# Kernel tuning notes

Measured on AMD Instinct MI355X. Metric: run time of the kernel, lower is better.

## Reference

```python
import jax, jax.numpy as jnp
import numpy as np

# Static cluster layout: B graphs, PER atoms each; first NIN are 'inside'
# (aux_ind==0), remaining NOUT are 'outside' periodic images (aux_ind==1).
B, PER, NIN, K = 256, 1024, 256, 32
NOUT = PER - NIN
N = B * PER
R = 6.0        # cutoff radius (Angstrom)
BOX = 32.0     # box side -> ~30 neighbors within R at this density


def setup_inputs() -> dict:
    key = jax.random.key(0)
    pos = jax.random.uniform(key, (N, 3), dtype=jnp.float32) * BOX
    batch = (jnp.arange(N, dtype=jnp.int32) // PER)
    aux_ind = ((jnp.arange(N, dtype=jnp.int32) % PER) >= NIN).astype(jnp.int32)
    return {"pos": pos, "batch": batch, "aux_ind": aux_ind}


def _select_neighbors(d, valid, k):
    """Pick up to k valid candidates per target, lowest candidate index first.
    d: [..., C] distances, valid: [..., C] bool. Returns (idx, mask, dist),
    each [..., k]; padded slots have mask=False and dist=0."""
    C = d.shape[-1]
    order_key = jnp.where(valid, jnp.arange(C, dtype=jnp.int32), C + 1)
    idx = jnp.argsort(order_key, axis=-1)[..., :k]          # [..., k]
    mask = jnp.take_along_axis(valid, idx, axis=-1)
    dist = jnp.where(mask, jnp.take_along_axis(d, idx, axis=-1), 0.0)
    return idx.astype(jnp.int32), mask, dist


def reference(pos, batch, aux_ind):
    # batch/aux_ind are encoded by the static contiguous layout above;
    # they parameterize the same structure torch builds via scatter_add/cumsum.
    pg = pos.reshape(B, PER, 3)
    ins = pg[:, :NIN]            # [B, NIN, 3]  inside (target + intra-conv) nodes
    outs = pg[:, NIN:]           # [B, NOUT, 3] outside (inter-conv) nodes

    # intra edges: inside -> inside, same graph, no self loops
    d_ii = jnp.sqrt(jnp.sum((ins[:, :, None, :] - ins[:, None, :, :]) ** 2, -1))  # [B,NIN,NIN]
    valid_ii = (d_ii < R) & ~jnp.eye(NIN, dtype=bool)
    idx_ii, m_ii, dist_ii = _select_neighbors(d_ii, valid_ii, K)

    # inter edges: outside -> inside, same graph
    d_io = jnp.sqrt(jnp.sum((ins[:, :, None, :] - outs[:, None, :, :]) ** 2, -1))  # [B,NIN,NOUT]
    valid_io = d_io < R
    idx_io, m_io, dist_io = _select_neighbors(d_io, valid_io, K)

    # relabel to global node indices (flow='source_to_target': row=source, col=target)
    goff = (jnp.arange(B, dtype=jnp.int32) * PER)[:, None, None]       # [B,1,1]
    tgt = jnp.broadcast_to(goff + jnp.arange(NIN, dtype=jnp.int32)[None, :, None],
                           (B, NIN, K))
    src_ii = goff + idx_ii
    src_io = goff + NIN + idx_io

    edge_index = jnp.stack([src_ii.reshape(-1), tgt.reshape(-1)], 0)        # [2, B*NIN*K]
    edge_index_inter = jnp.stack([src_io.reshape(-1), tgt.reshape(-1)], 0)  # [2, B*NIN*K]

    return (edge_index, m_ii.reshape(-1), dist_ii,
            edge_index_inter, m_io.reshape(-1), dist_io)
```

## Files before the change

kernel.cpp:

```cpp
#include <hip/hip_runtime.h>
#include <math.h>


constexpr int BB    = 256;
constexpr int PERN  = 1024;
constexpr int NINC  = 256;
constexpr int NOUTC = 768;
constexpr int KK    = 32;
constexpr long EE   = (long)BB * NINC * KK;

__device__ __forceinline__ int prefix_lt(unsigned long long m) {
    return __builtin_amdgcn_mbcnt_hi((unsigned)(m >> 32),
           __builtin_amdgcn_mbcnt_lo((unsigned)m, 0u));
}

__global__ __launch_bounds__(256) void mo3e_ballot_kernel(const float* __restrict__ pos,
                                                          float* __restrict__ out) {
#pragma clang fp contract(off)
    __shared__ float4 sp[PERN];

    const int b      = blockIdx.x >> 6;
    const int i_base = (blockIdx.x & 63) * 4;
    const int tid    = threadIdx.x;
    const int w      = tid >> 6;
    const int l      = tid & 63;

    const float* gp = pos + (long)b * PERN * 3;
    for (int idx = tid; idx < PERN; idx += 256) {
        sp[idx] = make_float4(gp[idx * 3 + 0], gp[idx * 3 + 1], gp[idx * 3 + 2], 0.0f);
    }
    __syncthreads();

    const int i = i_base + w;
    const float4 p = sp[i];
    const float xi = p.x, yi = p.y, zi = p.z;

    const int  goff = b * PERN;
    const long e0   = ((long)(b * NINC + i)) * KK;

    float* __restrict__ o_src_ii = out;
    float* __restrict__ o_tgt_ii = out + EE;
    float* __restrict__ o_m_ii   = out + 2 * EE;
    float* __restrict__ o_d_ii   = out + 3 * EE;
    float* __restrict__ o_src_io = out + 4 * EE;
    float* __restrict__ o_tgt_io = out + 5 * EE;
    float* __restrict__ o_m_io   = out + 6 * EE;
    float* __restrict__ o_d_io   = out + 7 * EE;

    const float tv = (float)(goff + i);
    if (l < KK) {
        o_tgt_ii[e0 + l] = tv;
        o_tgt_io[e0 + l] = tv;
    }

    {
        int cnt = 0;
        for (int it = 0; it < NINC / 64; ++it) {
            const int j = it * 64 + l;
            const float4 q = sp[j];
            const float dx = xi - q.x, dy = yi - q.y, dz = zi - q.z;
            const float d2 = (dx * dx + dy * dy) + dz * dz;
            const bool valid = (d2 < 36.0f) && (j != i);
            const unsigned long long ms = __ballot(valid);
            const int slot = cnt + prefix_lt(ms);
            if (valid && slot < KK) {
                o_src_ii[e0 + slot] = (float)(goff + j);
                o_d_ii[e0 + slot]   = sqrtf(d2);
            }
            cnt += __popcll(ms);
            cnt = __builtin_amdgcn_readfirstlane(cnt);
            if (cnt >= KK) break;
        }
        const int S0 = cnt < KK ? cnt : KK;
        if (l < KK) {
            o_m_ii[e0 + l] = (l < S0) ? 1.0f : 0.0f;
            if (l >= S0) o_d_ii[e0 + l] = 0.0f;
        }
        if (S0 < KK) {
            int pc = S0;
            for (int it = 0; it < NINC / 64; ++it) {
                const int j = it * 64 + l;
                const float4 q = sp[j];
                const float dx = xi - q.x, dy = yi - q.y, dz = zi - q.z;
                const float d2 = (dx * dx + dy * dy) + dz * dz;
                const bool inv = !((d2 < 36.0f) && (j != i));
                const unsigned long long ms = __ballot(inv);
                const int slot = pc + prefix_lt(ms);
                if (inv && slot < KK) o_src_ii[e0 + slot] = (float)(goff + j);
                pc += __popcll(ms);
                pc = __builtin_amdgcn_readfirstlane(pc);
                if (pc >= KK) break;
            }
        }
    }

    {
        int cnt = 0;
        for (int it = 0; it < NOUTC / 64; ++it) {
            const int c = NINC + it * 64 + l;
            const float4 q = sp[c];
            const float dx = xi - q.x, dy = yi - q.y, dz = zi - q.z;
            const float d2 = (dx * dx + dy * dy) + dz * dz;
            const bool valid = (d2 < 36.0f);
            const unsigned long long ms = __ballot(valid);
            const int slot = cnt + prefix_lt(ms);
            if (valid && slot < KK) {
                o_src_io[e0 + slot] = (float)(goff + c);
                o_d_io[e0 + slot]   = sqrtf(d2);
            }
            cnt += __popcll(ms);
            cnt = __builtin_amdgcn_readfirstlane(cnt);
            if (cnt >= KK) break;
        }
        const int S0 = cnt < KK ? cnt : KK;
        if (l < KK) {
            o_m_io[e0 + l] = (l < S0) ? 1.0f : 0.0f;
            if (l >= S0) o_d_io[e0 + l] = 0.0f;
        }
        if (S0 < KK) {
            int pc = S0;
            for (int it = 0; it < NOUTC / 64; ++it) {
                const int c = NINC + it * 64 + l;
                const float4 q = sp[c];
                const float dx = xi - q.x, dy = yi - q.y, dz = zi - q.z;
                const float d2 = (dx * dx + dy * dy) + dz * dz;
                const bool inv = !(d2 < 36.0f);
                const unsigned long long ms = __ballot(inv);
                const int slot = pc + prefix_lt(ms);
                if (inv && slot < KK) o_src_io[e0 + slot] = (float)(goff + c);
                pc += __popcll(ms);
                pc = __builtin_amdgcn_readfirstlane(pc);
                if (pc >= KK) break;
            }
        }
    }
}

extern "C" void kernel_launch(void* const* d_in, const int* in_sizes, int n_in,
                              void* d_out, int out_size, void* d_ws, size_t ws_size,
                              hipStream_t stream) {
    const float* pos = (const float*)d_in[0];
    float* out = (float*)d_out;

    mo3e_ballot_kernel<<<dim3(BB * 64), dim3(256), 0, stream>>>(pos, out);
}
```

Measured before the change: 126.5 us.

## Use 1024-thread blocks, cache ballot masks for padding pass, use fast sqrt

Blocks grow to 1024 threads handling 16 targets each, so each graph's positions are staged into shared memory 4x fewer times per graph. The padding pass now reuses the ballot masks saved during the first pass instead of recomputing distances. It also switches to the hardware sqrt intrinsic, keeps the target index wave-uniform, and removes the self-loop test from the per-lane predicate by clearing one bit of the ballot. Risks are lower occupancy flexibility with large blocks and possible sqrt precision differences.

```diff
diff --git a/kernel.cpp b/kernel.cpp
--- a/kernel.cpp
+++ b/kernel.cpp
@@ -14,122 +14,120 @@
            __builtin_amdgcn_mbcnt_lo((unsigned)m, 0u));
 }
 
-__global__ __launch_bounds__(256) void mo3e_ballot_kernel(const float* __restrict__ pos,
-                                                          float* __restrict__ out) {
+__device__ __forceinline__ float fast_sqrt(float x) {
+    return __builtin_amdgcn_sqrtf(x);
+}
+
+__global__ __launch_bounds__(1024) void mo3e_kernel(const float* __restrict__ pos,
+                                                    float* __restrict__ out) {
 #pragma clang fp contract(off)
     __shared__ float4 sp[PERN];
 
-    const int b      = blockIdx.x >> 6;
-    const int i_base = (blockIdx.x & 63) * 4;
-    const int tid    = threadIdx.x;
-    const int w      = tid >> 6;
-    const int l      = tid & 63;
+    const int b   = blockIdx.x >> 4;
+    const int tid = threadIdx.x;
+    const int l   = tid & 63;
+    const int i = __builtin_amdgcn_readfirstlane((blockIdx.x & 15) * 16 + (tid >> 6));
 
     const float* gp = pos + (long)b * PERN * 3;
-    for (int idx = tid; idx < PERN; idx += 256) {
-        sp[idx] = make_float4(gp[idx * 3 + 0], gp[idx * 3 + 1], gp[idx * 3 + 2], 0.0f);
-    }
+    sp[tid] = make_float4(gp[tid * 3 + 0], gp[tid * 3 + 1], gp[tid * 3 + 2], 0.0f);
     __syncthreads();
 
-    const int i = i_base + w;
     const float4 p = sp[i];
     const float xi = p.x, yi = p.y, zi = p.z;
 
     const int  goff = b * PERN;
     const long e0   = ((long)(b * NINC + i)) * KK;
 
-    float* __restrict__ o_src_ii = out;
-    float* __restrict__ o_tgt_ii = out + EE;
-    float* __restrict__ o_m_ii   = out + 2 * EE;
-    float* __restrict__ o_d_ii   = out + 3 * EE;
-    float* __restrict__ o_src_io = out + 4 * EE;
-    float* __restrict__ o_tgt_io = out + 5 * EE;
-    float* __restrict__ o_m_io   = out + 6 * EE;
-    float* __restrict__ o_d_io   = out + 7 * EE;
+    float* __restrict__ p_src_ii = out + e0;
+    float* __restrict__ p_tgt_ii = out + EE + e0;
+    float* __restrict__ p_m_ii   = out + 2 * EE + e0;
+    float* __restrict__ p_d_ii   = out + 3 * EE + e0;
+    float* __restrict__ p_src_io = out + 4 * EE + e0;
+    float* __restrict__ p_tgt_io = out + 5 * EE + e0;
+    float* __restrict__ p_m_io   = out + 6 * EE + e0;
+    float* __restrict__ p_d_io   = out + 7 * EE + e0;
 
+    const float fl = (float)l;
     const float tv = (float)(goff + i);
     if (l < KK) {
-        o_tgt_ii[e0 + l] = tv;
-        o_tgt_io[e0 + l] = tv;
+        p_tgt_ii[l] = tv;
+        p_tgt_io[l] = tv;
     }
 
     {
+        unsigned long long masks[NINC / 64];
         int cnt = 0;
+#pragma unroll
         for (int it = 0; it < NINC / 64; ++it) {
             const int j = it * 64 + l;
             const float4 q = sp[j];
             const float dx = xi - q.x, dy = yi - q.y, dz = zi - q.z;
             const float d2 = (dx * dx + dy * dy) + dz * dz;
-            const bool valid = (d2 < 36.0f) && (j != i);
-            const unsigned long long ms = __ballot(valid);
+            unsigned long long ms = __ballot(d2 < 36.0f);
+            if (it == (i >> 6)) ms &= ~(1ull << (i & 63));
+            masks[it] = ms;
             const int slot = cnt + prefix_lt(ms);
-            if (valid && slot < KK) {
-                o_src_ii[e0 + slot] = (float)(goff + j);
-                o_d_ii[e0 + slot]   = sqrtf(d2);
+            const bool mine = (ms >> l) & 1ull;
+            if (mine && slot < KK) {
+                p_src_ii[slot] = (float)(goff + it * 64) + fl;
+                p_d_ii[slot]   = fast_sqrt(d2);
             }
             cnt += __popcll(ms);
-            cnt = __builtin_amdgcn_readfirstlane(cnt);
             if (cnt >= KK) break;
         }
         const int S0 = cnt < KK ? cnt : KK;
         if (l < KK) {
-            o_m_ii[e0 + l] = (l < S0) ? 1.0f : 0.0f;
-            if (l >= S0) o_d_ii[e0 + l] = 0.0f;
+            p_m_ii[l] = (l < S0) ? 1.0f : 0.0f;
+            if (l >= S0) p_d_ii[l] = 0.0f;
         }
         if (S0 < KK) {
             int pc = S0;
+#pragma unroll
             for (int it = 0; it < NINC / 64; ++it) {
-                const int j = it * 64 + l;
-                const float4 q = sp[j];
-                const float dx = xi - q.x, dy = yi - q.y, dz = zi - q.z;
-                const float d2 = (dx * dx + dy * dy) + dz * dz;
-                const bool inv = !((d2 < 36.0f) && (j != i));
-                const unsigned long long ms = __ballot(inv);
-                const int slot = pc + prefix_lt(ms);
-                if (inv && slot < KK) o_src_ii[e0 + slot] = (float)(goff + j);
-                pc += __popcll(ms);
-                pc = __builtin_amdgcn_readfirstlane(pc);
+                const unsigned long long inv = ~masks[it];
+                const int slot = pc + prefix_lt(inv);
+                const bool mine = (inv >> l) & 1ull;
+                if (mine && slot < KK) p_src_ii[slot] = (float)(goff + it * 64) + fl;
+                pc += __popcll(inv);
                 if (pc >= KK) break;
             }
         }
     }
 
     {
+        unsigned long long masks[NOUTC / 64];
         int cnt = 0;
+#pragma unroll
         for (int it = 0; it < NOUTC / 64; ++it) {
             const int c = NINC + it * 64 + l;
             const float4 q = sp[c];
             const float dx = xi - q.x, dy = yi - q.y, dz = zi - q.z;
             const float d2 = (dx * dx + dy * dy) + dz * dz;
-            const bool valid = (d2 < 36.0f);
-            const unsigned long long ms = __ballot(valid);
+            const unsigned long long ms = __ballot(d2 < 36.0f);
+            masks[it] = ms;
             const int slot = cnt + prefix_lt(ms);
-            if (valid && slot < KK) {
-                o_src_io[e0 + slot] = (float)(goff + c);
-                o_d_io[e0 + slot]   = sqrtf(d2);
+            const bool mine = (ms >> l) & 1ull;
+            if (mine && slot < KK) {
+                p_src_io[slot] = (float)(goff + NINC + it * 64) + fl;
+                p_d_io[slot]   = fast_sqrt(d2);
             }
             cnt += __popcll(ms);
-            cnt = __builtin_amdgcn_readfirstlane(cnt);
             if (cnt >= KK) break;
         }
         const int S0 = cnt < KK ? cnt : KK;
         if (l < KK) {
-            o_m_io[e0 + l] = (l < S0) ? 1.0f : 0.0f;
-            if (l >= S0) o_d_io[e0 + l] = 0.0f;
+            p_m_io[l] = (l < S0) ? 1.0f : 0.0f;
+            if (l >= S0) p_d_io[l] = 0.0f;
         }
         if (S0 < KK) {
             int pc = S0;
+#pragma unroll
             for (int it = 0; it < NOUTC / 64; ++it) {
-                const int c = NINC + it * 64 + l;
-                const float4 q = sp[c];
-                const float dx = xi - q.x, dy = yi - q.y, dz = zi - q.z;
-                const float d2 = (dx * dx + dy * dy) + dz * dz;
-                const bool inv = !(d2 < 36.0f);
-                const unsigned long long ms = __ballot(inv);
-                const int slot = pc + prefix_lt(ms);
-                if (inv && slot < KK) o_src_io[e0 + slot] = (float)(goff + c);
-                pc += __popcll(ms);
-                pc = __builtin_amdgcn_readfirstlane(pc);
+                const unsigned long long inv = ~masks[it];
+                const int slot = pc + prefix_lt(inv);
+                const bool mine = (inv >> l) & 1ull;
+                if (mine && slot < KK) p_src_io[slot] = (float)(goff + NINC + it * 64) + fl;
+                pc += __popcll(inv);
                 if (pc >= KK) break;
             }
         }
@@ -142,5 +140,5 @@
     const float* pos = (const float*)d_in[0];
     float* out = (float*)d_out;
 
-    mo3e_ballot_kernel<<<dim3(BB * 64), dim3(256), 0, stream>>>(pos, out);
+    mo3e_kernel<<<dim3(BB * 16), dim3(1024), 0, stream>>>(pos, out);
 }
```

Result: faster. 110.4 us (-12.8%).
